# Optimization experiments

Hardware: AMD Instinct MI355X
Metric: run time of the kernel (lower is better)

The kernel has to match this reference:

```python
import jax, jax.numpy as jnp
import numpy as np

V, E, H, B, T = 50257, 300, 512, 4, 512  # vocab, embed(300 fixed), hid_size, batch, max_seq_len


def setup_inputs() -> dict:
    key = jax.random.key(0)
    ks = jax.random.split(key, 12)
    n = lambda k, shp, s: jax.random.normal(k, shp, dtype=jnp.float32) * s
    return {
        "tokens": jax.random.randint(ks[0], (B, T), 0, V),
        "emb_table": n(ks[1], (V, E), 0.02),      # frozen pretrained embedding
        # forward-direction LstmCellWithProjection params (cell_size == hidden_size == H)
        "W_ih_f": n(ks[2], (E, 4 * H), 0.05),     # input_linearity (no bias)
        "W_hh_f": n(ks[3], (H, 4 * H), 0.05),     # state_linearity weight
        "b_f": jnp.zeros((4 * H,), jnp.float32),  # state_linearity bias
        "W_proj_f": n(ks[4], (H, H), 0.05),       # state_projection (no bias)
        # backward direction
        "W_ih_b": n(ks[5], (E, 4 * H), 0.05),
        "W_hh_b": n(ks[6], (H, 4 * H), 0.05),
        "b_b": jnp.zeros((4 * H,), jnp.float32),
        "W_proj_b": n(ks[7], (H, H), 0.05),
        # final vocab projection nn.Linear(H, V)
        "W_lin": n(ks[8], (H, V), 0.02),
        "b_lin": jnp.zeros((V,), jnp.float32),
    }


def _lstm_proj_scan(x, W_ih, W_hh, b, W_proj):
    """ElmoLstm's LstmCellWithProjection over time. x: [B,T,E] -> [B,T,H]."""
    xp = jnp.einsum("bte,eg->btg", x, W_ih)  # precompute input projections [B,T,4H]

    def step(carry, xt):  # xt: [B,4H]
        h, c = carry
        p = xt + h @ W_hh + b
        i = jax.nn.sigmoid(p[:, :H])
        f = jax.nn.sigmoid(p[:, H:2 * H])
        g = jnp.tanh(p[:, 2 * H:3 * H])
        o = jax.nn.sigmoid(p[:, 3 * H:])
        c2 = i * g + f * c
        h2 = (o * jnp.tanh(c2)) @ W_proj  # projected hidden state
        return (h2, c2), h2

    init = (jnp.zeros((x.shape[0], H), x.dtype), jnp.zeros((x.shape[0], H), x.dtype))
    _, hs = jax.lax.scan(step, init, jnp.swapaxes(xp, 0, 1))  # [T,B,H]
    return jnp.swapaxes(hs, 0, 1)  # [B,T,H]


def reference(tokens, emb_table, W_ih_f, W_hh_f, b_f, W_proj_f,
              W_ih_b, W_hh_b, b_b, W_proj_b, W_lin, b_lin):
    x = emb_table[tokens]  # embedding gather [B,T,E]
    fwd = _lstm_proj_scan(x, W_ih_f, W_hh_f, b_f, W_proj_f)
    bwd = _lstm_proj_scan(x[:, ::-1], W_ih_b, W_hh_b, b_b, W_proj_b)[:, ::-1]
    # num_layers == 1 -> enc is (1,B,T,2H); fwd half / bwd half each through shared Linear
    logits_fwd = (fwd @ W_lin + b_lin).reshape(-1, V)  # [B*T, V]
    logits_bwd = (bwd @ W_lin + b_lin).reshape(-1, V)
    return jnp.concatenate([logits_fwd, logits_bwd], axis=0)  # [2*B*T, V]
```

## Files before the change

### kernel.cpp

```cpp
#include <hip/hip_runtime.h>
#include <hip/hip_bf16.h>

typedef unsigned short u16;
typedef unsigned int u32;
typedef unsigned long long u64;
typedef short bf16x8 __attribute__((ext_vector_type(8)));
typedef float f32x4 __attribute__((ext_vector_type(4)));

#define AS1C(p) ((const __attribute__((address_space(1))) void*)(p))
#define AS3(p)  ((__attribute__((address_space(3))) void*)(p))

__device__ __forceinline__ u16 f2bf(float f) {
    union { float f; unsigned u; } v; v.f = f;
    unsigned x = v.u;
    unsigned r = (x + 0x7FFFu + ((x >> 16) & 1u)) >> 16;
    return (u16)r;
}
__device__ __forceinline__ void st_atomic_u32(u32* p, u32 v) {
    __hip_atomic_store(p, v, __ATOMIC_RELAXED, __HIP_MEMORY_SCOPE_AGENT);
}
__device__ __forceinline__ u32 ld_atomic_u32(const u32* p) {
    return __hip_atomic_load(p, __ATOMIC_RELAXED, __HIP_MEMORY_SCOPE_AGENT);
}

__device__ __forceinline__ void tpose_dev(float (*tile)[33],
        const float* __restrict__ in, u16* __restrict__ out,
        int R, int C, int outR, int ldO, int bx, int by, int atomicStore) {
    int c0 = bx * 32, r0 = by * 32;
    int tx = threadIdx.x & 31, ty = threadIdx.x >> 5;
#pragma unroll
    for (int yy = 0; yy < 4; ++yy) {
        int r = r0 + ty + yy * 8, cc = c0 + tx;
        tile[ty + yy * 8][tx] = (r < R && cc < C) ? in[(size_t)r * C + cc] : 0.f;
    }
    __syncthreads();
#pragma unroll
    for (int yy = 0; yy < 4; ++yy) {
        int c = c0 + ty + yy * 8, r = r0 + tx;
        float v = tile[tx][ty + yy * 8];
        if (atomicStore) {
            float pv = __shfl_down(v, 1);
            if ((tx & 1) == 0 && c < outR && r < ldO)
                st_atomic_u32((u32*)&out[(size_t)c * ldO + r], (u32)f2bf(v) | ((u32)f2bf(pv) << 16));
        } else {
            if (c < outR && r < ldO) out[(size_t)c * ldO + r] = f2bf(v);
        }
    }
    __syncthreads();
}

__global__ __launch_bounds__(256) void prep(
    const int* __restrict__ tokens, const float* __restrict__ emb, u16* __restrict__ xemb,
    const float* __restrict__ W_ih_f, u16* __restrict__ WT_ihf,
    const float* __restrict__ W_ih_b, u16* __restrict__ WT_ihb,
    const float* __restrict__ W_hh_f, u16* __restrict__ WT_hhf,
    const float* __restrict__ W_hh_b, u16* __restrict__ WT_hhb,
    const float* __restrict__ W_proj_f, u16* __restrict__ WprojTf,
    const float* __restrict__ W_proj_b, u16* __restrict__ WprojTb,
    u16* __restrict__ WprojAf, u16* __restrict__ WprojAb,
    const float* __restrict__ W_lin, u16* __restrict__ WT_lin,
    u64* __restrict__ htag, u32* __restrict__ ctr)
{
    __shared__ float tile[32][33];
    int bid = blockIdx.x;
    int tid = threadIdx.x;
    if (bid < 2048) {
        int tok = tokens[bid];
        const float* src = emb + (size_t)tok * 300;
        u16* dst = xemb + (size_t)bid * 320;
        int c = tid;
        if (c < 320) dst[c] = (c < 300) ? f2bf(src[c]) : (u16)0;
        c += 256;
        if (c < 320) dst[c] = (c < 300) ? f2bf(src[c]) : (u16)0;
        return;
    }
    bid -= 2048;
    if (bid < 640)  { tpose_dev(tile, W_ih_f, WT_ihf, 300, 2048, 2048, 320, bid % 64, bid / 64, 0); return; }
    bid -= 640;
    if (bid < 640)  { tpose_dev(tile, W_ih_b, WT_ihb, 300, 2048, 2048, 320, bid % 64, bid / 64, 0); return; }
    bid -= 640;
    if (bid < 1024) { tpose_dev(tile, W_hh_f, WT_hhf, 512, 2048, 2048, 512, bid % 64, bid / 64, 0); return; }
    bid -= 1024;
    if (bid < 1024) { tpose_dev(tile, W_hh_b, WT_hhb, 512, 2048, 2048, 512, bid % 64, bid / 64, 0); return; }
    bid -= 1024;
    if (bid < 256)  { tpose_dev(tile, W_proj_f, WprojTf, 512, 512, 512, 512, bid % 16, bid / 16, 0); return; }
    bid -= 256;
    if (bid < 256)  { tpose_dev(tile, W_proj_b, WprojTb, 512, 512, 512, 512, bid % 16, bid / 16, 0); return; }
    bid -= 256;
    if (bid < 512)  { int i = bid * 512 + tid; WprojAf[i] = f2bf(W_proj_f[i]); WprojAf[i + 256] = f2bf(W_proj_f[i + 256]); return; }
    bid -= 512;
    if (bid < 512)  { int i = bid * 512 + tid; WprojAb[i] = f2bf(W_proj_b[i]); WprojAb[i + 256] = f2bf(W_proj_b[i + 256]); return; }
    bid -= 512;
    if (bid < 25152) { tpose_dev(tile, W_lin, WT_lin, 512, 50257, 50304, 512, bid % 1572, bid / 1572, 0); return; }
    for (int i = tid; i < 2 * 2 * 4 * 256; i += 256) htag[i] = 0ull;
    if (tid < 64) ctr[tid] = 0;
}

struct GemmJob {
    const u16* A; const u16* BT; float* Cf; u16* Cb; const float* bias;
    int M, Nreal, K, ldA, ldB, ldC, arev, orev, orow_base;
};

__device__ __forceinline__ void gemm_body(const GemmJob& j, int m0, int n0,
                                          char* As, char* Bs, int atomicCb) {
    const int tid = threadIdx.x;
    const int lane = tid & 63;
    const int wid = tid >> 6;
    const int wr = wid >> 1, wc = wid & 1;

    f32x4 zero4 = {0.f, 0.f, 0.f, 0.f};
    f32x4 acc[4][4];
#pragma unroll
    for (int i = 0; i < 4; ++i)
#pragma unroll
        for (int jx = 0; jx < 4; ++jx) acc[i][jx] = zero4;

    const int kIters = j.K >> 5;
    const int l15 = lane & 15, kg = lane >> 4;

    const int srow0 = wid * 32 + (lane >> 2);
    const int srow1 = srow0 + 16;
    const int c0 = (lane & 3) ^ (srow0 & 3);
    const int c1 = (lane & 3) ^ (srow1 & 3);
    int ar0 = m0 + srow0, ar1 = m0 + srow1;
    if (j.arev) {
        ar0 = (ar0 & ~511) | (511 - (ar0 & 511));
        ar1 = (ar1 & ~511) | (511 - (ar1 & 511));
    }
    const u16* ga0 = j.A + (size_t)ar0 * j.ldA + c0 * 8;
    const u16* ga1 = j.A + (size_t)ar1 * j.ldA + c1 * 8;
    const u16* gb0 = j.BT + (size_t)(n0 + srow0) * j.ldB + c0 * 8;
    const u16* gb1 = j.BT + (size_t)(n0 + srow1) * j.ldB + c1 * 8;
    char* ldsA0 = As + wid * 2048;
    char* ldsA1 = As + wid * 2048 + 1024;
    char* ldsB0 = Bs + wid * 2048;
    char* ldsB1 = Bs + wid * 2048 + 1024;

    for (int kt = 0; kt < kIters; ++kt) {
// ... 23 lines not shown
        __syncthreads();
    }

#pragma unroll
    for (int nt = 0; nt < 4; ++nt) {
        int col = n0 + wc * 64 + nt * 16 + l15;
        float bv = (j.bias != nullptr && col < j.Nreal) ? j.bias[col] : 0.f;
#pragma unroll
        for (int mt = 0; mt < 4; ++mt) {
#pragma unroll
            for (int jx = 0; jx < 4; ++jx) {
                int m = m0 + wr * 64 + mt * 16 + kg * 4 + jx;
                int om = j.orev ? ((m & ~511) | (511 - (m & 511))) : m;
                om += j.orow_base;
                float v = acc[mt][nt][jx] + bv;
                if (atomicCb) {
                    float pv = __shfl_down(v, 1);
                    if ((l15 & 1) == 0 && col < j.Nreal)
                        st_atomic_u32((u32*)(j.Cb + (size_t)om * j.ldC + col),
                                      (u32)f2bf(v) | ((u32)f2bf(pv) << 16));
                } else if (col < j.Nreal) {
                    if (j.Cf) j.Cf[(size_t)om * j.ldC + col] = v;
                    else      j.Cb[(size_t)om * j.ldC + col] = f2bf(v);
                }
            }
        }
    }
}

__global__ __launch_bounds__(256) void gemm_multi4(GemmJob j0, GemmJob j1, GemmJob j2, GemmJob j3) {
    __shared__ char pool[16384];
    GemmJob j = (blockIdx.z == 0) ? j0 : (blockIdx.z == 1) ? j1 : (blockIdx.z == 2) ? j2 : j3;
    if ((int)blockIdx.y * 128 >= j.M) return;
    gemm_body(j, blockIdx.y * 128, blockIdx.x * 128, pool, pool + 8192, 0);
}

__global__ __launch_bounds__(256) void lstm_fused(
    const float* __restrict__ Wc_f, const float* __restrict__ Wc_b,
    const float* __restrict__ xp_f, const float* __restrict__ xp_b,
    u64* __restrict__ htag,
    u16* __restrict__ hpre_f, u16* __restrict__ hpre_b,
    const u16* __restrict__ WT_lin,
    const u16* __restrict__ WprojTf, const u16* __restrict__ WprojTb,
    u16* __restrict__ hall, const float* __restrict__ b_lin,
    float* __restrict__ out, u32* __restrict__ ctr)
{
    __shared__ char pool[16384];
    const int tid = threadIdx.x;
    int bid = blockIdx.x;

    if (bid >= 64) {
        bid -= 64;
        if (bid < 128) {
            int dir = bid >> 6, r = bid & 63, y = r >> 2, x = r & 3;
            int m0 = y * 128, n0 = x * 128;
            if (tid == 0) {
                while (ld_atomic_u32(&ctr[8 + dir * 4 + (y & 3)]) < 32u) __builtin_amdgcn_s_sleep(32);
            }
            __syncthreads();
            GemmJob j = { dir ? hpre_b : hpre_f, dir ? WprojTb : WprojTf, nullptr, hall, nullptr,
                          2048, 512, 512, 512, 512, 512, 0, dir ? 1 : 0, dir ? 2048 : 0 };
            gemm_body(j, m0, n0, pool, pool + 8192, 1);
            asm volatile("s_waitcnt vmcnt(0)" ::: "memory");
            __syncthreads();
            if (tid == 0) {
                int obrow = j.orow_base + (j.orev ? ((m0 & ~511) | (511 - ((m0 + 127) & 511))) : m0);
                __hip_atomic_fetch_add(&ctr[16 + (obrow >> 7)], 1u, __ATOMIC_RELAXED, __HIP_MEMORY_SCOPE_AGENT);
            }
            return;
        }
        bid -= 128;
        {
            int cid = bid / (393 * 8), rr = bid % (393 * 8), bi = rr / 393, x = rr % 393;
            int band = (bi < 4) ? (bi * 4 + cid) : (16 + (bi - 4) * 4 + (3 - cid));
            if (tid == 0) {
                while (ld_atomic_u32(&ctr[16 + band]) < 4u) __builtin_amdgcn_s_sleep(127);
            }
            __syncthreads();
            GemmJob j = { hall, WT_lin, out, nullptr, b_lin,
                          4096, 50257, 512, 512, 512, 50257, 0, 0, 0 };
            gemm_body(j, band * 128, x * 128, pool, pool + 8192, 0);
            return;
        }
    }

    __builtin_amdgcn_s_setprio(1);
    u16 (*hlds)[520] = (u16(*)[520])pool;
    float (*gsum)[4][16] = (float(*)[4][16])(pool + 4160);
    float (*cbuf)[16] = (float(*)[16])(pool + 5184);

    const int dir = blockIdx.x >> 5;
    const int blk = blockIdx.x & 31;
    const int lane = tid & 63;
    const int wid = tid >> 6;
    const int l15 = lane & 15;
    const int kg = lane >> 4;

    const float* wcsrc = dir ? Wc_b : Wc_f;
    const float* xp    = dir ? xp_b : xp_f;
    u16* hpre          = dir ? hpre_b : hpre_f;
    u64* ht            = htag + (size_t)dir * 2 * 4 * 256;

    bf16x8 wcf[16];
#pragma unroll
    for (int ks = 0; ks < 16; ++ks) {
        bf16x8 w;
#pragma unroll
        for (int e = 0; e < 8; ++e) {
            int k = ks * 32 + kg * 8 + e;
            w[e] = (short)f2bf(wcsrc[(size_t)k * 2048 + wid * 512 + blk * 16 + l15]);
        }
        wcf[ks] = w;
    }
    if (tid < 64) cbuf[tid >> 4][tid & 15] = 0.f;
    __syncthreads();

    const bf16x8 zero8 = {0, 0, 0, 0, 0, 0, 0, 0};
    const int b = tid >> 4, hu = tid & 15;

    for (int t = 0; t < 512; ++t) {
        float xpv0 = 0.f, xpv1 = 0.f, xpv2 = 0.f, xpv3 = 0.f;
        if (tid < 64) {
            const float* xr = xp + ((size_t)(b * 512 + t)) * 2048 + blk * 16 + hu;
            xpv0 = xr[0]; xpv1 = xr[512]; xpv2 = xr[1024]; xpv3 = xr[1536];
        }
        {
            const u64* src = ht + (size_t)(t & 1) * 4 * 256;
            const u64* p0 = src + tid;
            const u64* p1 = src + 256 + tid;
            const u64* p2 = src + 512 + tid;
            const u64* p3 = src + 768 + tid;
            const u32 target = (u32)t;
            u64 w0, w1, w2, w3;
            for (;;) {
                asm volatile(
                    "global_load_dwordx2 %0, %4, off sc0 sc1\n\t"
                    "global_load_dwordx2 %1, %5, off sc0 sc1\n\t"
                    "global_load_dwordx2 %2, %6, off sc0 sc1\n\t"
                    "global_load_dwordx2 %3, %7, off sc0 sc1\n\t"
                    "s_waitcnt vmcnt(0)"
                    : "=&v"(w0), "=&v"(w1), "=&v"(w2), "=&v"(w3)
                    : "v"(p0), "v"(p1), "v"(p2), "v"(p3)
                    : "memory");
                if (((u32)(w0 >> 32) == target) & ((u32)(w1 >> 32) == target) &
                    ((u32)(w2 >> 32) == target) & ((u32)(w3 >> 32) == target)) break;
                __builtin_amdgcn_s_sleep(1);
            }
            asm volatile("" ::: "memory");
            *(u32*)&hlds[0][tid * 2] = (u32)w0;
            *(u32*)&hlds[1][tid * 2] = (u32)w1;
            *(u32*)&hlds[2][tid * 2] = (u32)w2;
            *(u32*)&hlds[3][tid * 2] = (u32)w3;
        }
        __syncthreads();

        f32x4 a0 = {0,0,0,0}, a1 = {0,0,0,0}, a2 = {0,0,0,0}, a3 = {0,0,0,0};
#pragma unroll
        for (int ks = 0; ks < 16; ++ks) {
            bf16x8 a = zero8;
            if (l15 < 4) a = *(const bf16x8*)&hlds[l15][ks * 32 + kg * 8];
            switch (ks & 3) {
                case 0: a0 = __builtin_amdgcn_mfma_f32_16x16x32_bf16(a, wcf[ks], a0, 0, 0, 0); break;
                case 1: a1 = __builtin_amdgcn_mfma_f32_16x16x32_bf16(a, wcf[ks], a1, 0, 0, 0); break;
                case 2: a2 = __builtin_amdgcn_mfma_f32_16x16x32_bf16(a, wcf[ks], a2, 0, 0, 0); break;
                default: a3 = __builtin_amdgcn_mfma_f32_16x16x32_bf16(a, wcf[ks], a3, 0, 0, 0); break;
            }
        }
        f32x4 accs = (a0 + a1) + (a2 + a3);
        if (lane < 16) {
#pragma unroll
            for (int jx = 0; jx < 4; ++jx) gsum[wid][jx][lane] = accs[jx];
        }
        __syncthreads();

        if (tid < 64) {
            float pi = xpv0 + gsum[0][b][hu];
            float pf = xpv1 + gsum[1][b][hu];
            float pg = xpv2 + gsum[2][b][hu];
            float po = xpv3 + gsum[3][b][hu];
            float iv = 1.f / (1.f + expf(-pi));
            float fv = 1.f / (1.f + expf(-pf));
            float gv = tanhf(pg);
            float ov = 1.f / (1.f + expf(-po));
            float c2 = iv * gv + fv * cbuf[b][hu];
            cbuf[b][hu] = c2;
            u16 hpb = f2bf(ov * tanhf(c2));
            unsigned v = hpb;
            unsigned nb = (unsigned)__shfl_down((int)v, 1);
            if ((tid & 1) == 0) {
                u32 packed = v | (nb << 16);
                u64 val = ((u64)(u32)(t + 1) << 32) | (u64)packed;
                size_t idx = (size_t)(((t + 1) & 1) * 4 + b) * 256 + blk * 8 + (hu >> 1);
                __hip_atomic_store(&ht[idx], val, __ATOMIC_RELAXED, __HIP_MEMORY_SCOPE_AGENT);
                st_atomic_u32((u32*)&hpre[(size_t)(b * 512 + t) * 512 + blk * 16 + hu], packed);
            }
        }
        if ((t & 127) == 127) {
            if (tid < 64) { asm volatile("s_waitcnt vmcnt(0)" ::: "memory"); }
            if (tid == 0)
                __hip_atomic_fetch_add(&ctr[8 + dir * 4 + (t >> 7)], 1u,
                                       __ATOMIC_RELAXED, __HIP_MEMORY_SCOPE_AGENT);
        }
    }
}

extern "C" void kernel_launch(void* const* d_in, const int* in_sizes, int n_in,
                              void* d_out, int out_size, void* d_ws, size_t ws_size,
                              hipStream_t stream) {
    const int*   tokens   = (const int*)d_in[0];
    const float* emb      = (const float*)d_in[1];
    const float* W_ih_f   = (const float*)d_in[2];
    const float* W_hh_f   = (const float*)d_in[3];
    const float* b_f      = (const float*)d_in[4];
    const float* W_proj_f = (const float*)d_in[5];
    const float* W_ih_b   = (const float*)d_in[6];
    const float* W_hh_b   = (const float*)d_in[7];
    const float* b_b      = (const float*)d_in[8];
    const float* W_proj_b = (const float*)d_in[9];
    const float* W_lin    = (const float*)d_in[10];
    const float* b_lin    = (const float*)d_in[11];
    float* out = (float*)d_out;

    char* ws = (char*)d_ws;
    size_t off = 0;
    auto alloc = [&](size_t bytes) -> char* {
        char* p = ws + off;
        off = (off + bytes + 255) & ~(size_t)255;
        return p;
    };
    u16* xemb     = (u16*)alloc(2048 * 320 * 2);
    u16* WT_ihf   = (u16*)alloc(2048 * 320 * 2);
    u16* WT_ihb   = (u16*)alloc(2048 * 320 * 2);
    u16* WT_hhf   = (u16*)alloc(2048 * 512 * 2);
    u16* WT_hhb   = (u16*)alloc(2048 * 512 * 2);
    u16* WprojTf  = (u16*)alloc(512 * 512 * 2);
    u16* WprojTb  = (u16*)alloc(512 * 512 * 2);
    u16* WprojAf  = (u16*)alloc(512 * 512 * 2);
    u16* WprojAb  = (u16*)alloc(512 * 512 * 2);
    u16* WT_lin   = (u16*)alloc((size_t)50304 * 512 * 2);
    float* xpf    = (float*)alloc((size_t)2048 * 2048 * 4);
    float* xpb    = (float*)alloc((size_t)2048 * 2048 * 4);
    float* Wc32f  = (float*)alloc((size_t)512 * 2048 * 4);
    float* Wc32b  = (float*)alloc((size_t)512 * 2048 * 4);
    u16* hpref    = (u16*)alloc((size_t)2048 * 512 * 2);
    u16* hpreb    = (u16*)alloc((size_t)2048 * 512 * 2);
    u16* hall     = (u16*)alloc((size_t)4096 * 512 * 2);
    u64* htag     = (u64*)alloc((size_t)2 * 2 * 4 * 256 * 8);
    u32* ctr      = (u32*)alloc(64 * 4);

    prep<<<2048 + 640 + 640 + 1024 + 1024 + 256 + 256 + 512 + 512 + 25152 + 1, 256, 0, stream>>>(
        tokens, emb, xemb,
        W_ih_f, WT_ihf, W_ih_b, WT_ihb,
        W_hh_f, WT_hhf, W_hh_b, WT_hhb,
        W_proj_f, WprojTf, W_proj_b, WprojTb,
        WprojAf, WprojAb, W_lin, WT_lin, htag, ctr);

    GemmJob jxf = {xemb, WT_ihf, xpf, nullptr, b_f, 2048, 2048, 320, 320, 320, 2048, 0, 0, 0};
    GemmJob jxb = {xemb, WT_ihb, xpb, nullptr, b_b, 2048, 2048, 320, 320, 320, 2048, 1, 0, 0};
    GemmJob jwf = {WprojAf, WT_hhf, Wc32f, nullptr, nullptr, 512, 2048, 512, 512, 512, 2048, 0, 0, 0};
    GemmJob jwb = {WprojAb, WT_hhb, Wc32b, nullptr, nullptr, 512, 2048, 512, 512, 512, 2048, 0, 0, 0};
    gemm_multi4<<<dim3(16, 16, 4), 256, 0, stream>>>(jxf, jxb, jwf, jwb);

    lstm_fused<<<64 + 128 + 12576, 256, 0, stream>>>(
        Wc32f, Wc32b, xpf, xpb, htag, hpref, hpreb,
        WT_lin, WprojTf, WprojTb, hall, b_lin, out, ctr);
}
```

Before: 1.663 ms.

## Remap LSTM blocks onto one XCD and poll a local-cache tag buffer

Remaps block indices so each LSTM direction's 32 recurrent blocks land on the same XCD (assuming round-robin dispatch by blockIdx mod 8), interleaving the projection and logits blocks on the remaining slots. Each step's hidden-state tags are now written twice, with a plain store to a local buffer and an agent-scope atomic to a global buffer. Consumers poll the local buffer with sc0 only, avoiding the sc1 bypass of L2, and fall back to the global buffer permanently if 64 polls fail. The aim is lower per-step cross-block sync latency. It depends on an undocumented XCD placement assumption and adds an extra store per step.

```diff
diff --git a/kernel.cpp b/kernel.cpp
--- a/kernel.cpp
+++ b/kernel.cpp
@@ -25,7 +25,7 @@
 
 __device__ __forceinline__ void tpose_dev(float (*tile)[33],
         const float* __restrict__ in, u16* __restrict__ out,
-        int R, int C, int outR, int ldO, int bx, int by, int atomicStore) {
+        int R, int C, int outR, int ldO, int bx, int by) {
     int c0 = bx * 32, r0 = by * 32;
     int tx = threadIdx.x & 31, ty = threadIdx.x >> 5;
 #pragma unroll
@@ -37,14 +37,7 @@
 #pragma unroll
     for (int yy = 0; yy < 4; ++yy) {
         int c = c0 + ty + yy * 8, r = r0 + tx;
-        float v = tile[tx][ty + yy * 8];
-        if (atomicStore) {
-            float pv = __shfl_down(v, 1);
-            if ((tx & 1) == 0 && c < outR && r < ldO)
-                st_atomic_u32((u32*)&out[(size_t)c * ldO + r], (u32)f2bf(v) | ((u32)f2bf(pv) << 16));
-        } else {
-            if (c < outR && r < ldO) out[(size_t)c * ldO + r] = f2bf(v);
-        }
+        if (c < outR && r < ldO) out[(size_t)c * ldO + r] = f2bf(tile[tx][ty + yy * 8]);
     }
     __syncthreads();
 }
@@ -59,7 +52,7 @@
     const float* __restrict__ W_proj_b, u16* __restrict__ WprojTb,
     u16* __restrict__ WprojAf, u16* __restrict__ WprojAb,
     const float* __restrict__ W_lin, u16* __restrict__ WT_lin,
-    u64* __restrict__ htag, u32* __restrict__ ctr)
+    u64* __restrict__ htagG, u64* __restrict__ htagL, u32* __restrict__ ctr)
 {
     __shared__ float tile[32][33];
     int bid = blockIdx.x;
@@ -75,24 +68,24 @@
         return;
     }
     bid -= 2048;
-    if (bid < 640)  { tpose_dev(tile, W_ih_f, WT_ihf, 300, 2048, 2048, 320, bid % 64, bid / 64, 0); return; }
+    if (bid < 640)  { tpose_dev(tile, W_ih_f, WT_ihf, 300, 2048, 2048, 320, bid % 64, bid / 64); return; }
     bid -= 640;
-    if (bid < 640)  { tpose_dev(tile, W_ih_b, WT_ihb, 300, 2048, 2048, 320, bid % 64, bid / 64, 0); return; }
+    if (bid < 640)  { tpose_dev(tile, W_ih_b, WT_ihb, 300, 2048, 2048, 320, bid % 64, bid / 64); return; }
     bid -= 640;
-    if (bid < 1024) { tpose_dev(tile, W_hh_f, WT_hhf, 512, 2048, 2048, 512, bid % 64, bid / 64, 0); return; }
+    if (bid < 1024) { tpose_dev(tile, W_hh_f, WT_hhf, 512, 2048, 2048, 512, bid % 64, bid / 64); return; }
     bid -= 1024;
-    if (bid < 1024) { tpose_dev(tile, W_hh_b, WT_hhb, 512, 2048, 2048, 512, bid % 64, bid / 64, 0); return; }
+    if (bid < 1024) { tpose_dev(tile, W_hh_b, WT_hhb, 512, 2048, 2048, 512, bid % 64, bid / 64); return; }
     bid -= 1024;
-    if (bid < 256)  { tpose_dev(tile, W_proj_f, WprojTf, 512, 512, 512, 512, bid % 16, bid / 16, 0); return; }
+    if (bid < 256)  { tpose_dev(tile, W_proj_f, WprojTf, 512, 512, 512, 512, bid % 16, bid / 16); return; }
     bid -= 256;
-    if (bid < 256)  { tpose_dev(tile, W_proj_b, WprojTb, 512, 512, 512, 512, bid % 16, bid / 16, 0); return; }
+    if (bid < 256)  { tpose_dev(tile, W_proj_b, WprojTb, 512, 512, 512, 512, bid % 16, bid / 16); return; }
     bid -= 256;
     if (bid < 512)  { int i = bid * 512 + tid; WprojAf[i] = f2bf(W_proj_f[i]); WprojAf[i + 256] = f2bf(W_proj_f[i + 256]); return; }
     bid -= 512;
     if (bid < 512)  { int i = bid * 512 + tid; WprojAb[i] = f2bf(W_proj_b[i]); WprojAb[i + 256] = f2bf(W_proj_b[i + 256]); return; }
     bid -= 512;
-    if (bid < 25152) { tpose_dev(tile, W_lin, WT_lin, 512, 50257, 50304, 512, bid % 1572, bid / 1572, 0); return; }
-    for (int i = tid; i < 2 * 2 * 4 * 256; i += 256) htag[i] = 0ull;
+    if (bid < 25152) { tpose_dev(tile, W_lin, WT_lin, 512, 50257, 50304, 512, bid % 1572, bid / 1572); return; }
+    for (int i = tid; i < 2 * 2 * 4 * 256; i += 256) { htagG[i] = 0ull; htagL[i] = 0ull; }
     if (tid < 64) ctr[tid] = 0;
 }
 
@@ -199,7 +192,7 @@
 __global__ __launch_bounds__(256) void lstm_fused(
     const float* __restrict__ Wc_f, const float* __restrict__ Wc_b,
     const float* __restrict__ xp_f, const float* __restrict__ xp_b,
-    u64* __restrict__ htag,
+    u64* __restrict__ htagG, u64* __restrict__ htagL,
     u16* __restrict__ hpre_f, u16* __restrict__ hpre_b,
     const u16* __restrict__ WT_lin,
     const u16* __restrict__ WprojTf, const u16* __restrict__ WprojTb,
@@ -208,31 +201,37 @@
 {
     __shared__ char pool[16384];
     const int tid = threadIdx.x;
-    int bid = blockIdx.x;
-
-    if (bid >= 64) {
-        bid -= 64;
-        if (bid < 128) {
-            int dir = bid >> 6, r = bid & 63, y = r >> 2, x = r & 3;
-            int m0 = y * 128, n0 = x * 128;
-            if (tid == 0) {
-                while (ld_atomic_u32(&ctr[8 + dir * 4 + (y & 3)]) < 32u) __builtin_amdgcn_s_sleep(32);
-            }
-            __syncthreads();
-            GemmJob j = { dir ? hpre_b : hpre_f, dir ? WprojTb : WprojTf, nullptr, hall, nullptr,
-                          2048, 512, 512, 512, 512, 512, 0, dir ? 1 : 0, dir ? 2048 : 0 };
-            gemm_body(j, m0, n0, pool, pool + 8192, 1);
-            asm volatile("s_waitcnt vmcnt(0)" ::: "memory");
-            __syncthreads();
-            if (tid == 0) {
-                int obrow = j.orow_base + (j.orev ? ((m0 & ~511) | (511 - ((m0 + 127) & 511))) : m0);
-                __hip_atomic_fetch_add(&ctr[16 + (obrow >> 7)], 1u, __ATOMIC_RELAXED, __HIP_MEMORY_SCOPE_AGENT);
-            }
-            return;
-        }
-        bid -= 128;
-        {
-            int cid = bid / (393 * 8), rr = bid % (393 * 8), bi = rr / 393, x = rr % 393;
+    const int bidx = blockIdx.x;
+
+    int dir, blk;
+    {
+        int lid = -1;
+        if (bidx < 256) {
+            int mod8 = bidx & 7, grp = bidx >> 3;
+            if (mod8 >= 6) lid = (mod8 - 6) * 32 + grp;
+            else if (mod8 >= 2) {
+                int pid = (mod8 - 2) * 32 + grp;
+                int pdir = pid >> 6, r = pid & 63, y = r >> 2, x = r & 3;
+                int m0 = y * 128, n0 = x * 128;
+                if (tid == 0) {
+                    while (ld_atomic_u32(&ctr[8 + pdir * 4 + (y & 3)]) < 32u) __builtin_amdgcn_s_sleep(32);
+                }
+                __syncthreads();
+                GemmJob j = { pdir ? hpre_b : hpre_f, pdir ? WprojTb : WprojTf, nullptr, hall, nullptr,
+                              2048, 512, 512, 512, 512, 512, 0, pdir ? 1 : 0, pdir ? 2048 : 0 };
+                gemm_body(j, m0, n0, pool, pool + 8192, 1);
+                asm volatile("s_waitcnt vmcnt(0)" ::: "memory");
+                __syncthreads();
+                if (tid == 0) {
+                    int obrow = j.orow_base + (j.orev ? ((m0 & ~511) | (511 - ((m0 + 127) & 511))) : m0);
+                    __hip_atomic_fetch_add(&ctr[16 + (obrow >> 7)], 1u, __ATOMIC_RELAXED, __HIP_MEMORY_SCOPE_AGENT);
+                }
+                return;
+            } else { dir = mod8; blk = grp; }
+        } else lid = 64 + (bidx - 256);
+
+        if (lid >= 0) {
+            int cid = lid / (393 * 8), rr = lid % (393 * 8), bi = rr / 393, x = rr % 393;
             int band = (bi < 4) ? (bi * 4 + cid) : (16 + (bi - 4) * 4 + (3 - cid));
             if (tid == 0) {
                 while (ld_atomic_u32(&ctr[16 + band]) < 4u) __builtin_amdgcn_s_sleep(127);
@@ -250,8 +249,6 @@
     float (*gsum)[4][16] = (float(*)[4][16])(pool + 4160);
     float (*cbuf)[16] = (float(*)[16])(pool + 5184);
 
-    const int dir = blockIdx.x >> 5;
-    const int blk = blockIdx.x & 31;
     const int lane = tid & 63;
     const int wid = tid >> 6;
     const int l15 = lane & 15;
@@ -260,7 +257,8 @@
     const float* wcsrc = dir ? Wc_b : Wc_f;
     const float* xp    = dir ? xp_b : xp_f;
     u16* hpre          = dir ? hpre_b : hpre_f;
-    u64* ht            = htag + (size_t)dir * 2 * 4 * 256;
+    u64* htg           = htagG + (size_t)dir * 2 * 4 * 256;
+    u64* htl           = htagL + (size_t)dir * 2 * 4 * 256;
 
     bf16x8 wcf[16];
 #pragma unroll
@@ -278,6 +276,7 @@
 
     const bf16x8 zero8 = {0, 0, 0, 0, 0, 0, 0, 0};
     const int b = tid >> 4, hu = tid & 15;
+    bool useLocal = true;
 
     for (int t = 0; t < 512; ++t) {
         float xpv0 = 0.f, xpv1 = 0.f, xpv2 = 0.f, xpv3 = 0.f;
@@ -286,26 +285,51 @@
             xpv0 = xr[0]; xpv1 = xr[512]; xpv2 = xr[1024]; xpv3 = xr[1536];
         }
         {
-            const u64* src = ht + (size_t)(t & 1) * 4 * 256;
-            const u64* p0 = src + tid;
-            const u64* p1 = src + 256 + tid;
-            const u64* p2 = src + 512 + tid;
-            const u64* p3 = src + 768 + tid;
             const u32 target = (u32)t;
             u64 w0, w1, w2, w3;
-            for (;;) {
-                asm volatile(
-                    "global_load_dwordx2 %0, %4, off sc0 sc1\n\t"
-                    "global_load_dwordx2 %1, %5, off sc0 sc1\n\t"
-                    "global_load_dwordx2 %2, %6, off sc0 sc1\n\t"
-                    "global_load_dwordx2 %3, %7, off sc0 sc1\n\t"
-                    "s_waitcnt vmcnt(0)"
-                    : "=&v"(w0), "=&v"(w1), "=&v"(w2), "=&v"(w3)
-                    : "v"(p0), "v"(p1), "v"(p2), "v"(p3)
-                    : "memory");
-                if (((u32)(w0 >> 32) == target) & ((u32)(w1 >> 32) == target) &
-                    ((u32)(w2 >> 32) == target) & ((u32)(w3 >> 32) == target)) break;
-                __builtin_amdgcn_s_sleep(1);
+            bool got = false;
+            if (useLocal) {
+                const u64* s = htl + (size_t)(t & 1) * 4 * 256;
+                const u64* q0 = s + tid;
+                const u64* q1 = s + 256 + tid;
+                const u64* q2 = s + 512 + tid;
+                const u64* q3 = s + 768 + tid;
+                for (int it = 0; it < 64; ++it) {
+                    asm volatile(
+                        "global_load_dwordx2 %0, %4, off sc0\n\t"
+                        "global_load_dwordx2 %1, %5, off sc0\n\t"
+                        "global_load_dwordx2 %2, %6, off sc0\n\t"
+                        "global_load_dwordx2 %3, %7, off sc0\n\t"
+                        "s_waitcnt vmcnt(0)"
+                        : "=&v"(w0), "=&v"(w1), "=&v"(w2), "=&v"(w3)
+                        : "v"(q0), "v"(q1), "v"(q2), "v"(q3)
+                        : "memory");
+                    if (((u32)(w0 >> 32) == target) & ((u32)(w1 >> 32) == target) &
+                        ((u32)(w2 >> 32) == target) & ((u32)(w3 >> 32) == target)) { got = true; break; }
+                    __builtin_amdgcn_s_sleep(1);
+                }
+                useLocal = got;
+            }
+            if (!got) {
+                const u64* s = htg + (size_t)(t & 1) * 4 * 256;
+                const u64* q0 = s + tid;
+                const u64* q1 = s + 256 + tid;
+                const u64* q2 = s + 512 + tid;
+                const u64* q3 = s + 768 + tid;
+                for (;;) {
+                    asm volatile(
+                        "global_load_dwordx2 %0, %4, off sc0 sc1\n\t"
+                        "global_load_dwordx2 %1, %5, off sc0 sc1\n\t"
+                        "global_load_dwordx2 %2, %6, off sc0 sc1\n\t"
+                        "global_load_dwordx2 %3, %7, off sc0 sc1\n\t"
+                        "s_waitcnt vmcnt(0)"
+                        : "=&v"(w0), "=&v"(w1), "=&v"(w2), "=&v"(w3)
+                        : "v"(q0), "v"(q1), "v"(q2), "v"(q3)
+                        : "memory");
+                    if (((u32)(w0 >> 32) == target) & ((u32)(w1 >> 32) == target) &
+                        ((u32)(w2 >> 32) == target) & ((u32)(w3 >> 32) == target)) break;
+                    __builtin_amdgcn_s_sleep(1);
+                }
             }
             asm volatile("" ::: "memory");
             *(u32*)&hlds[0][tid * 2] = (u32)w0;
@@ -352,7 +376,8 @@
                 u32 packed = v | (nb << 16);
                 u64 val = ((u64)(u32)(t + 1) << 32) | (u64)packed;
                 size_t idx = (size_t)(((t + 1) & 1) * 4 + b) * 256 + blk * 8 + (hu >> 1);
-                __hip_atomic_store(&ht[idx], val, __ATOMIC_RELAXED, __HIP_MEMORY_SCOPE_AGENT);
+                asm volatile("global_store_dwordx2 %0, %1, off" :: "v"(htl + idx), "v"(val) : "memory");
+                __hip_atomic_store(&htg[idx], val, __ATOMIC_RELAXED, __HIP_MEMORY_SCOPE_AGENT);
                 st_atomic_u32((u32*)&hpre[(size_t)(b * 512 + t) * 512 + blk * 16 + hu], packed);
             }
         }
@@ -406,7 +431,8 @@
     u16* hpref    = (u16*)alloc((size_t)2048 * 512 * 2);
     u16* hpreb    = (u16*)alloc((size_t)2048 * 512 * 2);
     u16* hall     = (u16*)alloc((size_t)4096 * 512 * 2);
-    u64* htag     = (u64*)alloc((size_t)2 * 2 * 4 * 256 * 8);
+    u64* htagG    = (u64*)alloc((size_t)2 * 2 * 4 * 256 * 8);
+    u64* htagL    = (u64*)alloc((size_t)2 * 2 * 4 * 256 * 8);
     u32* ctr      = (u32*)alloc(64 * 4);
 
     prep<<<2048 + 640 + 640 + 1024 + 1024 + 256 + 256 + 512 + 512 + 25152 + 1, 256, 0, stream>>>(
@@ -414,7 +440,7 @@
         W_ih_f, WT_ihf, W_ih_b, WT_ihb,
         W_hh_f, WT_hhf, W_hh_b, WT_hhb,
         W_proj_f, WprojTf, W_proj_b, WprojTb,
-        WprojAf, WprojAb, W_lin, WT_lin, htag, ctr);
+        WprojAf, WprojAb, W_lin, WT_lin, htagG, htagL, ctr);
 
     GemmJob jxf = {xemb, WT_ihf, xpf, nullptr, b_f, 2048, 2048, 320, 320, 320, 2048, 0, 0, 0};
     GemmJob jxb = {xemb, WT_ihb, xpb, nullptr, b_b, 2048, 2048, 320, 320, 320, 2048, 1, 0, 0};
@@ -422,7 +448,7 @@
     GemmJob jwb = {WprojAb, WT_hhb, Wc32b, nullptr, nullptr, 512, 2048, 512, 512, 512, 2048, 0, 0, 0};
     gemm_multi4<<<dim3(16, 16, 4), 256, 0, stream>>>(jxf, jxb, jwf, jwb);
 
-    lstm_fused<<<64 + 128 + 12576, 256, 0, stream>>>(
-        Wc32f, Wc32b, xpf, xpb, htag, hpref, hpreb,
+    lstm_fused<<<256 + 12576 - 64, 256, 0, stream>>>(
+        Wc32f, Wc32b, xpf, xpb, htagG, htagL, hpref, hpreb,
         WT_lin, WprojTf, WprojTb, hall, b_lin, out, ctr);
 }
```

After: 2.169 ms. +30.4%, slower.

## Widen fused LSTM blocks to 1024 threads, cutting recurrent workgroups per direction to eight

Applied to the files above, without the earlier changes.

The fused LSTM kernel now runs 1024-thread workgroups. Each recurrent block handles 64 hidden units, so each direction uses 8 blocks instead of 32, which cuts the number of cross-block handshake participants per timestep. The projection and vocab GEMM tiles are also packed four per workgroup, and the counter thresholds are adjusted to match. Each timestep's gate computation now serializes more work per block, and the larger blocks may lower occupancy for the vocab GEMM phase.

```diff
diff --git a/kernel.cpp b/kernel.cpp
--- a/kernel.cpp
+++ b/kernel.cpp
@@ -25,7 +25,7 @@
 
 __device__ __forceinline__ void tpose_dev(float (*tile)[33],
         const float* __restrict__ in, u16* __restrict__ out,
-        int R, int C, int outR, int ldO, int bx, int by, int atomicStore) {
+        int R, int C, int outR, int ldO, int bx, int by) {
     int c0 = bx * 32, r0 = by * 32;
     int tx = threadIdx.x & 31, ty = threadIdx.x >> 5;
 #pragma unroll
@@ -37,14 +37,7 @@
 #pragma unroll
     for (int yy = 0; yy < 4; ++yy) {
         int c = c0 + ty + yy * 8, r = r0 + tx;
-        float v = tile[tx][ty + yy * 8];
-        if (atomicStore) {
-            float pv = __shfl_down(v, 1);
-            if ((tx & 1) == 0 && c < outR && r < ldO)
-                st_atomic_u32((u32*)&out[(size_t)c * ldO + r], (u32)f2bf(v) | ((u32)f2bf(pv) << 16));
-        } else {
-            if (c < outR && r < ldO) out[(size_t)c * ldO + r] = f2bf(v);
-        }
+        if (c < outR && r < ldO) out[(size_t)c * ldO + r] = f2bf(tile[tx][ty + yy * 8]);
     }
     __syncthreads();
 }
@@ -75,23 +68,23 @@
         return;
     }
     bid -= 2048;
-    if (bid < 640)  { tpose_dev(tile, W_ih_f, WT_ihf, 300, 2048, 2048, 320, bid % 64, bid / 64, 0); return; }
+    if (bid < 640)  { tpose_dev(tile, W_ih_f, WT_ihf, 300, 2048, 2048, 320, bid % 64, bid / 64); return; }
     bid -= 640;
-    if (bid < 640)  { tpose_dev(tile, W_ih_b, WT_ihb, 300, 2048, 2048, 320, bid % 64, bid / 64, 0); return; }
+    if (bid < 640)  { tpose_dev(tile, W_ih_b, WT_ihb, 300, 2048, 2048, 320, bid % 64, bid / 64); return; }
     bid -= 640;
-    if (bid < 1024) { tpose_dev(tile, W_hh_f, WT_hhf, 512, 2048, 2048, 512, bid % 64, bid / 64, 0); return; }
+    if (bid < 1024) { tpose_dev(tile, W_hh_f, WT_hhf, 512, 2048, 2048, 512, bid % 64, bid / 64); return; }
     bid -= 1024;
-    if (bid < 1024) { tpose_dev(tile, W_hh_b, WT_hhb, 512, 2048, 2048, 512, bid % 64, bid / 64, 0); return; }
+    if (bid < 1024) { tpose_dev(tile, W_hh_b, WT_hhb, 512, 2048, 2048, 512, bid % 64, bid / 64); return; }
     bid -= 1024;
-    if (bid < 256)  { tpose_dev(tile, W_proj_f, WprojTf, 512, 512, 512, 512, bid % 16, bid / 16, 0); return; }
+    if (bid < 256)  { tpose_dev(tile, W_proj_f, WprojTf, 512, 512, 512, 512, bid % 16, bid / 16); return; }
     bid -= 256;
-    if (bid < 256)  { tpose_dev(tile, W_proj_b, WprojTb, 512, 512, 512, 512, bid % 16, bid / 16, 0); return; }
+    if (bid < 256)  { tpose_dev(tile, W_proj_b, WprojTb, 512, 512, 512, 512, bid % 16, bid / 16); return; }
     bid -= 256;
     if (bid < 512)  { int i = bid * 512 + tid; WprojAf[i] = f2bf(W_proj_f[i]); WprojAf[i + 256] = f2bf(W_proj_f[i + 256]); return; }
     bid -= 512;
     if (bid < 512)  { int i = bid * 512 + tid; WprojAb[i] = f2bf(W_proj_b[i]); WprojAb[i + 256] = f2bf(W_proj_b[i + 256]); return; }
     bid -= 512;
-    if (bid < 25152) { tpose_dev(tile, W_lin, WT_lin, 512, 50257, 50304, 512, bid % 1572, bid / 1572, 0); return; }
+    if (bid < 25152) { tpose_dev(tile, W_lin, WT_lin, 512, 50257, 50304, 512, bid % 1572, bid / 1572); return; }
     for (int i = tid; i < 2 * 2 * 4 * 256; i += 256) htag[i] = 0ull;
     if (tid < 64) ctr[tid] = 0;
 }
@@ -102,8 +95,7 @@
 };
 
 __device__ __forceinline__ void gemm_body(const GemmJob& j, int m0, int n0,
-                                          char* As, char* Bs, int atomicCb) {
-    const int tid = threadIdx.x;
+                                          char* As, char* Bs, int atomicCb, int tid) {
     const int lane = tid & 63;
     const int wid = tid >> 6;
     const int wr = wid >> 1, wc = wid & 1;
@@ -193,10 +185,10 @@
     __shared__ char pool[16384];
     GemmJob j = (blockIdx.z == 0) ? j0 : (blockIdx.z == 1) ? j1 : (blockIdx.z == 2) ? j2 : j3;
     if ((int)blockIdx.y * 128 >= j.M) return;
-    gemm_body(j, blockIdx.y * 128, blockIdx.x * 128, pool, pool + 8192, 0);
-}
-
-__global__ __launch_bounds__(256) void lstm_fused(
+    gemm_body(j, blockIdx.y * 128, blockIdx.x * 128, pool, pool + 8192, 0, threadIdx.x);
+}
+
+__global__ __launch_bounds__(1024) void lstm_fused(
     const float* __restrict__ Wc_f, const float* __restrict__ Wc_b,
     const float* __restrict__ xp_f, const float* __restrict__ xp_b,
     u64* __restrict__ htag,
@@ -206,54 +198,59 @@
     u16* __restrict__ hall, const float* __restrict__ b_lin,
     float* __restrict__ out, u32* __restrict__ ctr)
 {
-    __shared__ char pool[16384];
+    __shared__ char pool[65536];
     const int tid = threadIdx.x;
-    int bid = blockIdx.x;
-
-    if (bid >= 64) {
-        bid -= 64;
-        if (bid < 128) {
-            int dir = bid >> 6, r = bid & 63, y = r >> 2, x = r & 3;
-            int m0 = y * 128, n0 = x * 128;
+    const int bidx = blockIdx.x;
+
+    if (bidx >= 16) {
+        const int q = tid >> 8, tl = tid & 255;
+        char* As = pool + q * 16384;
+        char* Bs = As + 8192;
+        if (bidx < 48) {
+            int pid = bidx - 16;
+            int dir = pid >> 4, y = pid & 15;
             if (tid == 0) {
-                while (ld_atomic_u32(&ctr[8 + dir * 4 + (y & 3)]) < 32u) __builtin_amdgcn_s_sleep(32);
+                while (ld_atomic_u32(&ctr[8 + dir * 4 + (y & 3)]) < 8u) __builtin_amdgcn_s_sleep(32);
             }
             __syncthreads();
             GemmJob j = { dir ? hpre_b : hpre_f, dir ? WprojTb : WprojTf, nullptr, hall, nullptr,
                           2048, 512, 512, 512, 512, 512, 0, dir ? 1 : 0, dir ? 2048 : 0 };
-            gemm_body(j, m0, n0, pool, pool + 8192, 1);
+            gemm_body(j, y * 128, q * 128, As, Bs, 1, tl);
             asm volatile("s_waitcnt vmcnt(0)" ::: "memory");
             __syncthreads();
             if (tid == 0) {
-                int obrow = j.orow_base + (j.orev ? ((m0 & ~511) | (511 - ((m0 + 127) & 511))) : m0);
-                __hip_atomic_fetch_add(&ctr[16 + (obrow >> 7)], 1u, __ATOMIC_RELAXED, __HIP_MEMORY_SCOPE_AGENT);
+                int outband = dir ? (16 + (y & ~3) + (3 - (y & 3))) : y;
+                __hip_atomic_fetch_add(&ctr[16 + outband], 1u, __ATOMIC_RELAXED, __HIP_MEMORY_SCOPE_AGENT);
             }
             return;
         }
-        bid -= 128;
         {
-            int cid = bid / (393 * 8), rr = bid % (393 * 8), bi = rr / 393, x = rr % 393;
+            int lid = bidx - 48;
+            int cid = lid / 792, rr = lid % 792, bi = rr / 99, xblk = rr % 99;
             int band = (bi < 4) ? (bi * 4 + cid) : (16 + (bi - 4) * 4 + (3 - cid));
             if (tid == 0) {
-                while (ld_atomic_u32(&ctr[16 + band]) < 4u) __builtin_amdgcn_s_sleep(127);
+                while (ld_atomic_u32(&ctr[16 + band]) < 1u) __builtin_amdgcn_s_sleep(127);
             }
             __syncthreads();
+            int xt = xblk * 4 + q; if (xt > 392) xt = 392;
             GemmJob j = { hall, WT_lin, out, nullptr, b_lin,
                           4096, 50257, 512, 512, 512, 50257, 0, 0, 0 };
-            gemm_body(j, band * 128, x * 128, pool, pool + 8192, 0);
+            gemm_body(j, band * 128, xt * 128, As, Bs, 0, tl);
             return;
         }
     }
 
     __builtin_amdgcn_s_setprio(1);
-    u16 (*hlds)[520] = (u16(*)[520])pool;
+    u16 (*hlds)[520]     = (u16(*)[520])pool;
     float (*gsum)[4][16] = (float(*)[4][16])(pool + 4160);
-    float (*cbuf)[16] = (float(*)[16])(pool + 5184);
-
-    const int dir = blockIdx.x >> 5;
-    const int blk = blockIdx.x & 31;
+    float (*cbuf)[64]    = (float(*)[64])(pool + 8256);
+
+    const int dir = bidx >> 3;
+    const int blk = bidx & 7;
     const int lane = tid & 63;
-    const int wid = tid >> 6;
+    const int w = tid >> 6;
+    const int g = w >> 2;
+    const int cg = w & 3;
     const int l15 = lane & 15;
     const int kg = lane >> 4;
 
@@ -263,55 +260,46 @@
     u64* ht            = htag + (size_t)dir * 2 * 4 * 256;
 
     bf16x8 wcf[16];
-#pragma unroll
-    for (int ks = 0; ks < 16; ++ks) {
-        bf16x8 w;
-#pragma unroll
-        for (int e = 0; e < 8; ++e) {
-            int k = ks * 32 + kg * 8 + e;
-            w[e] = (short)f2bf(wcsrc[(size_t)k * 2048 + wid * 512 + blk * 16 + l15]);
-        }
-        wcf[ks] = w;
-    }
-    if (tid < 64) cbuf[tid >> 4][tid & 15] = 0.f;
+    {
+        const int wccol = g * 512 + blk * 64 + cg * 16 + l15;
+#pragma unroll
+        for (int ks = 0; ks < 16; ++ks) {
+            bf16x8 wv;
+#pragma unroll
+            for (int e = 0; e < 8; ++e) {
+                int k = ks * 32 + kg * 8 + e;
+                wv[e] = (short)f2bf(wcsrc[(size_t)k * 2048 + wccol]);
+            }
+            wcf[ks] = wv;
+        }
+    }
+    if (tid < 256) cbuf[tid >> 6][tid & 63] = 0.f;
     __syncthreads();
 
     const bf16x8 zero8 = {0, 0, 0, 0, 0, 0, 0, 0};
-    const int b = tid >> 4, hu = tid & 15;
+    const int b = tid >> 6, hu = tid & 63;
+    const int pb = tid >> 8, pw = tid & 255;
 
     for (int t = 0; t < 512; ++t) {
         float xpv0 = 0.f, xpv1 = 0.f, xpv2 = 0.f, xpv3 = 0.f;
-        if (tid < 64) {
-            const float* xr = xp + ((size_t)(b * 512 + t)) * 2048 + blk * 16 + hu;
+        if (tid < 256) {
+            const float* xr = xp + ((size_t)(b * 512 + t)) * 2048 + blk * 64 + hu;
             xpv0 = xr[0]; xpv1 = xr[512]; xpv2 = xr[1024]; xpv3 = xr[1536];
         }
         {
-            const u64* src = ht + (size_t)(t & 1) * 4 * 256;
-            const u64* p0 = src + tid;
-            const u64* p1 = src + 256 + tid;
-            const u64* p2 = src + 512 + tid;
-            const u64* p3 = src + 768 + tid;
+            const u64* p = ht + (size_t)(t & 1) * 4 * 256 + pb * 256 + pw;
             const u32 target = (u32)t;
-            u64 w0, w1, w2, w3;
+            u64 wv;
             for (;;) {
                 asm volatile(
-                    "global_load_dwordx2 %0, %4, off sc0 sc1\n\t"
-                    "global_load_dwordx2 %1, %5, off sc0 sc1\n\t"
-                    "global_load_dwordx2 %2, %6, off sc0 sc1\n\t"
-                    "global_load_dwordx2 %3, %7, off sc0 sc1\n\t"
+                    "global_load_dwordx2 %0, %1, off sc0 sc1\n\t"
                     "s_waitcnt vmcnt(0)"
-                    : "=&v"(w0), "=&v"(w1), "=&v"(w2), "=&v"(w3)
-                    : "v"(p0), "v"(p1), "v"(p2), "v"(p3)
-                    : "memory");
-                if (((u32)(w0 >> 32) == target) & ((u32)(w1 >> 32) == target) &
-                    ((u32)(w2 >> 32) == target) & ((u32)(w3 >> 32) == target)) break;
+                    : "=&v"(wv) : "v"(p) : "memory");
+                if ((u32)(wv >> 32) == target) break;
                 __builtin_amdgcn_s_sleep(1);
             }
             asm volatile("" ::: "memory");
-            *(u32*)&hlds[0][tid * 2] = (u32)w0;
-            *(u32*)&hlds[1][tid * 2] = (u32)w1;
-            *(u32*)&hlds[2][tid * 2] = (u32)w2;
-            *(u32*)&hlds[3][tid * 2] = (u32)w3;
+            *(u32*)&hlds[pb][pw * 2] = (u32)wv;
         }
         __syncthreads();
 
@@ -330,15 +318,15 @@
         f32x4 accs = (a0 + a1) + (a2 + a3);
         if (lane < 16) {
 #pragma unroll
-            for (int jx = 0; jx < 4; ++jx) gsum[wid][jx][lane] = accs[jx];
+            for (int jx = 0; jx < 4; ++jx) gsum[w][jx][lane] = accs[jx];
         }
         __syncthreads();
 
-        if (tid < 64) {
-            float pi = xpv0 + gsum[0][b][hu];
-            float pf = xpv1 + gsum[1][b][hu];
-            float pg = xpv2 + gsum[2][b][hu];
-            float po = xpv3 + gsum[3][b][hu];
+        if (tid < 256) {
+            float pi = xpv0 + gsum[0 * 4 + (hu >> 4)][b][hu & 15];
+            float pf = xpv1 + gsum[1 * 4 + (hu >> 4)][b][hu & 15];
+            float pg = xpv2 + gsum[2 * 4 + (hu >> 4)][b][hu & 15];
+            float po = xpv3 + gsum[3 * 4 + (hu >> 4)][b][hu & 15];
             float iv = 1.f / (1.f + expf(-pi));
             float fv = 1.f / (1.f + expf(-pf));
             float gv = tanhf(pg);
@@ -348,16 +336,17 @@
             u16 hpb = f2bf(ov * tanhf(c2));
             unsigned v = hpb;
             unsigned nb = (unsigned)__shfl_down((int)v, 1);
-            if ((tid & 1) == 0) {
+            if ((hu & 1) == 0) {
                 u32 packed = v | (nb << 16);
                 u64 val = ((u64)(u32)(t + 1) << 32) | (u64)packed;
-                size_t idx = (size_t)(((t + 1) & 1) * 4 + b) * 256 + blk * 8 + (hu >> 1);
+                size_t idx = (size_t)(((t + 1) & 1) * 4 + b) * 256 + blk * 32 + (hu >> 1);
                 __hip_atomic_store(&ht[idx], val, __ATOMIC_RELAXED, __HIP_MEMORY_SCOPE_AGENT);
-                st_atomic_u32((u32*)&hpre[(size_t)(b * 512 + t) * 512 + blk * 16 + hu], packed);
+                st_atomic_u32((u32*)&hpre[(size_t)(b * 512 + t) * 512 + blk * 64 + hu], packed);
             }
         }
         if ((t & 127) == 127) {
-            if (tid < 64) { asm volatile("s_waitcnt vmcnt(0)" ::: "memory"); }
+            if (tid < 256) { asm volatile("s_waitcnt vmcnt(0)" ::: "memory"); }
+            __syncthreads();
             if (tid == 0)
                 __hip_atomic_fetch_add(&ctr[8 + dir * 4 + (t >> 7)], 1u,
                                        __ATOMIC_RELAXED, __HIP_MEMORY_SCOPE_AGENT);
@@ -422,7 +411,7 @@
     GemmJob jwb = {WprojAb, WT_hhb, Wc32b, nullptr, nullptr, 512, 2048, 512, 512, 512, 2048, 0, 0, 0};
     gemm_multi4<<<dim3(16, 16, 4), 256, 0, stream>>>(jxf, jxb, jwf, jwb);
 
-    lstm_fused<<<64 + 128 + 12576, 256, 0, stream>>>(
+    lstm_fused<<<16 + 32 + 3168, 1024, 0, stream>>>(
         Wc32f, Wc32b, xpf, xpb, htag, hpref, hpreb,
         WT_lin, WprojTf, WprojTb, hall, b_lin, out, ctr);
 }
```

New measurement: 1.797 ms. 8.1% more time.

## Interleave gate columns per wave to remove per-step LDS reduction barrier

Applied to the files above, without the earlier changes.

The recurrent step now assigns weight columns so that each quad of MFMA output lanes holds the four gates of one hidden unit. The gate combine then runs in registers through lane shuffles instead of a shared-memory gsum exchange and a second __syncthreads per timestep. Cell state moves to registers, activations use exp2/rcp intrinsics, and the h buffer in LDS is double-buffered so the next step's writes don't race with the current step's reads. All waves now do the activation work redundantly, and the fast-math activations may slightly change numerics. The unused atomic-store path in the transpose helper is also removed.

```diff
diff --git a/kernel.cpp b/kernel.cpp
--- a/kernel.cpp
+++ b/kernel.cpp
@@ -25,7 +25,7 @@
 
 __device__ __forceinline__ void tpose_dev(float (*tile)[33],
         const float* __restrict__ in, u16* __restrict__ out,
-        int R, int C, int outR, int ldO, int bx, int by, int atomicStore) {
+        int R, int C, int outR, int ldO, int bx, int by) {
     int c0 = bx * 32, r0 = by * 32;
     int tx = threadIdx.x & 31, ty = threadIdx.x >> 5;
 #pragma unroll
@@ -37,14 +37,7 @@
 #pragma unroll
     for (int yy = 0; yy < 4; ++yy) {
         int c = c0 + ty + yy * 8, r = r0 + tx;
-        float v = tile[tx][ty + yy * 8];
-        if (atomicStore) {
-            float pv = __shfl_down(v, 1);
-            if ((tx & 1) == 0 && c < outR && r < ldO)
-                st_atomic_u32((u32*)&out[(size_t)c * ldO + r], (u32)f2bf(v) | ((u32)f2bf(pv) << 16));
-        } else {
-            if (c < outR && r < ldO) out[(size_t)c * ldO + r] = f2bf(v);
-        }
+        if (c < outR && r < ldO) out[(size_t)c * ldO + r] = f2bf(tile[tx][ty + yy * 8]);
     }
     __syncthreads();
 }
@@ -75,23 +68,23 @@
         return;
     }
     bid -= 2048;
-    if (bid < 640)  { tpose_dev(tile, W_ih_f, WT_ihf, 300, 2048, 2048, 320, bid % 64, bid / 64, 0); return; }
+    if (bid < 640)  { tpose_dev(tile, W_ih_f, WT_ihf, 300, 2048, 2048, 320, bid % 64, bid / 64); return; }
     bid -= 640;
-    if (bid < 640)  { tpose_dev(tile, W_ih_b, WT_ihb, 300, 2048, 2048, 320, bid % 64, bid / 64, 0); return; }
+    if (bid < 640)  { tpose_dev(tile, W_ih_b, WT_ihb, 300, 2048, 2048, 320, bid % 64, bid / 64); return; }
     bid -= 640;
-    if (bid < 1024) { tpose_dev(tile, W_hh_f, WT_hhf, 512, 2048, 2048, 512, bid % 64, bid / 64, 0); return; }
+    if (bid < 1024) { tpose_dev(tile, W_hh_f, WT_hhf, 512, 2048, 2048, 512, bid % 64, bid / 64); return; }
     bid -= 1024;
-    if (bid < 1024) { tpose_dev(tile, W_hh_b, WT_hhb, 512, 2048, 2048, 512, bid % 64, bid / 64, 0); return; }
+    if (bid < 1024) { tpose_dev(tile, W_hh_b, WT_hhb, 512, 2048, 2048, 512, bid % 64, bid / 64); return; }
     bid -= 1024;
-    if (bid < 256)  { tpose_dev(tile, W_proj_f, WprojTf, 512, 512, 512, 512, bid % 16, bid / 16, 0); return; }
+    if (bid < 256)  { tpose_dev(tile, W_proj_f, WprojTf, 512, 512, 512, 512, bid % 16, bid / 16); return; }
     bid -= 256;
-    if (bid < 256)  { tpose_dev(tile, W_proj_b, WprojTb, 512, 512, 512, 512, bid % 16, bid / 16, 0); return; }
+    if (bid < 256)  { tpose_dev(tile, W_proj_b, WprojTb, 512, 512, 512, 512, bid % 16, bid / 16); return; }
     bid -= 256;
     if (bid < 512)  { int i = bid * 512 + tid; WprojAf[i] = f2bf(W_proj_f[i]); WprojAf[i + 256] = f2bf(W_proj_f[i + 256]); return; }
     bid -= 512;
     if (bid < 512)  { int i = bid * 512 + tid; WprojAb[i] = f2bf(W_proj_b[i]); WprojAb[i + 256] = f2bf(W_proj_b[i + 256]); return; }
     bid -= 512;
-    if (bid < 25152) { tpose_dev(tile, W_lin, WT_lin, 512, 50257, 50304, 512, bid % 1572, bid / 1572, 0); return; }
+    if (bid < 25152) { tpose_dev(tile, W_lin, WT_lin, 512, 50257, 50304, 512, bid % 1572, bid / 1572); return; }
     for (int i = tid; i < 2 * 2 * 4 * 256; i += 256) htag[i] = 0ull;
     if (tid < 64) ctr[tid] = 0;
 }
@@ -246,16 +239,16 @@
     }
 
     __builtin_amdgcn_s_setprio(1);
-    u16 (*hlds)[520] = (u16(*)[520])pool;
-    float (*gsum)[4][16] = (float(*)[4][16])(pool + 4160);
-    float (*cbuf)[16] = (float(*)[16])(pool + 5184);
+    u16 (*hlds)[4][520] = (u16(*)[4][520])pool;
 
     const int dir = blockIdx.x >> 5;
     const int blk = blockIdx.x & 31;
     const int lane = tid & 63;
-    const int wid = tid >> 6;
+    const int w = tid >> 6;
     const int l15 = lane & 15;
     const int kg = lane >> 4;
+    const int gate = l15 & 3;
+    const int hloc = w * 4 + (l15 >> 2);
 
     const float* wcsrc = dir ? Wc_b : Wc_f;
     const float* xp    = dir ? xp_b : xp_f;
@@ -263,27 +256,29 @@
     u64* ht            = htag + (size_t)dir * 2 * 4 * 256;
 
     bf16x8 wcf[16];
-#pragma unroll
-    for (int ks = 0; ks < 16; ++ks) {
-        bf16x8 w;
-#pragma unroll
-        for (int e = 0; e < 8; ++e) {
-            int k = ks * 32 + kg * 8 + e;
-            w[e] = (short)f2bf(wcsrc[(size_t)k * 2048 + wid * 512 + blk * 16 + l15]);
-        }
-        wcf[ks] = w;
-    }
-    if (tid < 64) cbuf[tid >> 4][tid & 15] = 0.f;
-    __syncthreads();
+    {
+        const int wccol = gate * 512 + blk * 16 + hloc;
+#pragma unroll
+        for (int ks = 0; ks < 16; ++ks) {
+            bf16x8 wv;
+#pragma unroll
+            for (int e = 0; e < 8; ++e) {
+                int k = ks * 32 + kg * 8 + e;
+                wv[e] = (short)f2bf(wcsrc[(size_t)k * 2048 + wccol]);
+            }
+            wcf[ks] = wv;
+        }
+    }
 
     const bf16x8 zero8 = {0, 0, 0, 0, 0, 0, 0, 0};
-    const int b = tid >> 4, hu = tid & 15;
+    float cst[4] = {0.f, 0.f, 0.f, 0.f};
 
     for (int t = 0; t < 512; ++t) {
-        float xpv0 = 0.f, xpv1 = 0.f, xpv2 = 0.f, xpv3 = 0.f;
-        if (tid < 64) {
-            const float* xr = xp + ((size_t)(b * 512 + t)) * 2048 + blk * 16 + hu;
-            xpv0 = xr[0]; xpv1 = xr[512]; xpv2 = xr[1024]; xpv3 = xr[1536];
+        float xpv[4];
+        {
+            const float* xb = xp + (size_t)t * 2048 + gate * 512 + blk * 16 + hloc;
+#pragma unroll
+            for (int j = 0; j < 4; ++j) xpv[j] = xb[(size_t)j * 512 * 2048];
         }
         {
             const u64* src = ht + (size_t)(t & 1) * 4 * 256;
@@ -308,56 +303,66 @@
                 __builtin_amdgcn_s_sleep(1);
             }
             asm volatile("" ::: "memory");
-            *(u32*)&hlds[0][tid * 2] = (u32)w0;
-            *(u32*)&hlds[1][tid * 2] = (u32)w1;
-            *(u32*)&hlds[2][tid * 2] = (u32)w2;
-            *(u32*)&hlds[3][tid * 2] = (u32)w3;
+            *(u32*)&hlds[t & 1][0][tid * 2] = (u32)w0;
+            *(u32*)&hlds[t & 1][1][tid * 2] = (u32)w1;
+            *(u32*)&hlds[t & 1][2][tid * 2] = (u32)w2;
+            *(u32*)&hlds[t & 1][3][tid * 2] = (u32)w3;
         }
         __syncthreads();
 
-        f32x4 a0 = {0,0,0,0}, a1 = {0,0,0,0}, a2 = {0,0,0,0}, a3 = {0,0,0,0};
+        f32x4 a0 = {0, 0, 0, 0}, a1 = {0, 0, 0, 0};
 #pragma unroll
         for (int ks = 0; ks < 16; ++ks) {
             bf16x8 a = zero8;
-            if (l15 < 4) a = *(const bf16x8*)&hlds[l15][ks * 32 + kg * 8];
-            switch (ks & 3) {
-                case 0: a0 = __builtin_amdgcn_mfma_f32_16x16x32_bf16(a, wcf[ks], a0, 0, 0, 0); break;
-                case 1: a1 = __builtin_amdgcn_mfma_f32_16x16x32_bf16(a, wcf[ks], a1, 0, 0, 0); break;
-                case 2: a2 = __builtin_amdgcn_mfma_f32_16x16x32_bf16(a, wcf[ks], a2, 0, 0, 0); break;
-                default: a3 = __builtin_amdgcn_mfma_f32_16x16x32_bf16(a, wcf[ks], a3, 0, 0, 0); break;
-            }
-        }
-        f32x4 accs = (a0 + a1) + (a2 + a3);
-        if (lane < 16) {
-#pragma unroll
-            for (int jx = 0; jx < 4; ++jx) gsum[wid][jx][lane] = accs[jx];
-        }
-        __syncthreads();
-
-        if (tid < 64) {
-            float pi = xpv0 + gsum[0][b][hu];
-            float pf = xpv1 + gsum[1][b][hu];
-            float pg = xpv2 + gsum[2][b][hu];
-            float po = xpv3 + gsum[3][b][hu];
-            float iv = 1.f / (1.f + expf(-pi));
-            float fv = 1.f / (1.f + expf(-pf));
-            float gv = tanhf(pg);
-            float ov = 1.f / (1.f + expf(-po));
-            float c2 = iv * gv + fv * cbuf[b][hu];
-            cbuf[b][hu] = c2;
-            u16 hpb = f2bf(ov * tanhf(c2));
-            unsigned v = hpb;
-            unsigned nb = (unsigned)__shfl_down((int)v, 1);
-            if ((tid & 1) == 0) {
-                u32 packed = v | (nb << 16);
+            if (l15 < 4) a = *(const bf16x8*)&hlds[t & 1][l15][ks * 32 + kg * 8];
+            if (ks & 1) a1 = __builtin_amdgcn_mfma_f32_16x16x32_bf16(a, wcf[ks], a1, 0, 0, 0);
+            else        a0 = __builtin_amdgcn_mfma_f32_16x16x32_bf16(a, wcf[ks], a0, 0, 0, 0);
+        }
+        f32x4 accs = a0 + a1;
+
+        float act[4];
+#pragma unroll
+        for (int j = 0; j < 4; ++j) {
+            float x = accs[j] + xpv[j];
+            float m = (gate == 2) ? 2.885390082f : -1.442695041f;
+            float r = __builtin_amdgcn_rcpf(1.f + __builtin_amdgcn_exp2f(m * x));
+            act[j] = (gate == 2) ? (1.f - 2.f * r) : r;
+        }
+        const int base = lane & ~3;
+        float fv[4], gv[4], ov[4];
+#pragma unroll
+        for (int j = 0; j < 4; ++j) {
+            fv[j] = __shfl(act[j], base + 1);
+            gv[j] = __shfl(act[j], base + 2);
+            ov[j] = __shfl(act[j], base + 3);
+        }
+        unsigned hbits[4];
+#pragma unroll
+        for (int j = 0; j < 4; ++j) {
+            float c2 = act[j] * gv[j] + fv[j] * cst[j];
+            cst[j] = c2;
+            float th = 1.f - 2.f * __builtin_amdgcn_rcpf(1.f + __builtin_amdgcn_exp2f(2.885390082f * c2));
+            hbits[j] = f2bf(ov[j] * th);
+        }
+        unsigned pb4[4];
+#pragma unroll
+        for (int j = 0; j < 4; ++j) pb4[j] = (unsigned)__shfl((int)hbits[j], (lane + 4) & 63);
+
+        if ((lane & 7) == 0 && lane < 16) {
+            const int word = blk * 8 + w * 2 + (lane >> 3);
+            const int slot = (t + 1) & 1;
+#pragma unroll
+            for (int j = 0; j < 4; ++j) {
+                u32 packed = hbits[j] | (pb4[j] << 16);
                 u64 val = ((u64)(u32)(t + 1) << 32) | (u64)packed;
-                size_t idx = (size_t)(((t + 1) & 1) * 4 + b) * 256 + blk * 8 + (hu >> 1);
-                __hip_atomic_store(&ht[idx], val, __ATOMIC_RELAXED, __HIP_MEMORY_SCOPE_AGENT);
-                st_atomic_u32((u32*)&hpre[(size_t)(b * 512 + t) * 512 + blk * 16 + hu], packed);
+                __hip_atomic_store(&ht[(size_t)(slot * 4 + j) * 256 + word], val,
+                                   __ATOMIC_RELAXED, __HIP_MEMORY_SCOPE_AGENT);
+                st_atomic_u32((u32*)&hpre[(size_t)(j * 512 + t) * 512 + word * 2], packed);
             }
         }
         if ((t & 127) == 127) {
-            if (tid < 64) { asm volatile("s_waitcnt vmcnt(0)" ::: "memory"); }
+            asm volatile("s_waitcnt vmcnt(0)" ::: "memory");
+            __syncthreads();
             if (tid == 0)
                 __hip_atomic_fetch_add(&ctr[8 + dir * 4 + (t >> 7)], 1u,
                                        __ATOMIC_RELAXED, __HIP_MEMORY_SCOPE_AGENT);
```

Result: no change. 1.653 ms (-0.6%).
